# Optimization experiments

Hardware: AMD Instinct MI355X
Metric: run time of the kernel (lower is better)

## Reference

```python
import jax, jax.numpy as jnp
import numpy as np

B, S, D = 2, 2048, 2048
H, DH = 16, 128          # n_heads, head_dim
HFF = 8192               # hidden_dim (SwiGLU)
EPS = 1e-5               # layer_norm_eps passed to AdvancedRMSNorm


def setup_inputs() -> dict:
    key = jax.random.key(0)
    ks = jax.random.split(key, 16)
    sd = lambda fan_in: 1.0 / np.sqrt(fan_in)
    inp = {
        "x": jax.random.normal(ks[0], (B, S, D), jnp.float32),
        # attention (torch Linear weights: [out, in])
        "q_w": jax.random.normal(ks[1], (D, D), jnp.float32) * sd(D),
        "k_w": jax.random.normal(ks[2], (D, D), jnp.float32) * sd(D),
        "v_w": jax.random.normal(ks[3], (D, D), jnp.float32) * sd(D),
        "o_w": jax.random.normal(ks[4], (D, D), jnp.float32) * sd(D),
        "temp": jnp.ones((H, 1, 1), jnp.float32),  # learnable per-head temperature
        # RMSNorm scales
        "ln1_w": jnp.ones((D,), jnp.float32),
        "ln2_w": jnp.ones((D,), jnp.float32),
        # SwiGLU
        "gate_w": jax.random.normal(ks[5], (HFF, D), jnp.float32) * sd(D),
        "up_w": jax.random.normal(ks[6], (HFF, D), jnp.float32) * sd(D),
        "gate2_w": jax.random.normal(ks[7], (HFF, D), jnp.float32) * sd(D),
        "down_w": jax.random.normal(ks[8], (D, HFF), jnp.float32) * sd(HFF),
        # gated residual connections (Linear with bias)
        "ag_w": jax.random.normal(ks[9], (D, D), jnp.float32) * sd(D),
        "ag_b": jnp.zeros((D,), jnp.float32),
        "fg_w": jax.random.normal(ks[10], (D, D), jnp.float32) * sd(D),
        "fg_b": jnp.zeros((D,), jnp.float32),
    }
    return inp


def _rmsnorm(x, w):
    rms = jnp.sqrt(jnp.mean(x * x, axis=-1, keepdims=True) + EPS)
    return w * (x / rms)


def _l2norm(x):
    # F.normalize(dim=-1): x / max(||x||_2, 1e-12)
    n = jnp.sqrt(jnp.sum(x * x, axis=-1, keepdims=True))
    return x / jnp.maximum(n, 1e-12)


def _block(x, q_w, k_w, v_w, o_w, temp, ln1_w, ln2_w,
           gate_w, up_w, gate2_w, down_w, ag_w, ag_b, fg_w, fg_b):
    # --- cosine-sim attention sublayer ---
    residual = x
    h = _rmsnorm(x, ln1_w)
    q = (h @ q_w.T).reshape(B, S, H, DH).transpose(0, 2, 1, 3)  # [B,H,S,DH]
    k = (h @ k_w.T).reshape(B, S, H, DH).transpose(0, 2, 1, 3)
    v = (h @ v_w.T).reshape(B, S, H, DH).transpose(0, 2, 1, 3)
    q = _l2norm(q)
    k = _l2norm(k)
    scores = jnp.einsum("bhqd,bhkd->bhqk", q, k) * temp  # temp [H,1,1] broadcasts
    causal = jnp.triu(jnp.ones((S, S), bool), k=1)
    scores = jnp.where(causal, -jnp.inf, scores)
    attn = jax.nn.softmax(scores, axis=-1)
    out = jnp.einsum("bhqk,bhkd->bhqd", attn, v)
    out = out.transpose(0, 2, 1, 3).reshape(B, S, D)
    attn_out = out @ o_w.T
    # gated residual: sigmoid(W a + b)*a + (1-g)*residual
    g = jax.nn.sigmoid(attn_out @ ag_w.T + ag_b)
    x = g * attn_out + (1.0 - g) * residual
    # --- SwiGLU sublayer ---
    residual = x
    h = _rmsnorm(x, ln2_w)
    gate = jax.nn.silu(h @ gate_w.T)
    up = h @ up_w.T
    gate2 = jax.nn.sigmoid(h @ gate2_w.T)
    ffn_out = (gate * up * gate2) @ down_w.T
    g = jax.nn.sigmoid(ffn_out @ fg_w.T + fg_b)
    return g * ffn_out + (1.0 - g) * residual


def reference(x, q_w, k_w, v_w, o_w, temp, ln1_w, ln2_w,
              gate_w, up_w, gate2_w, down_w, ag_w, ag_b, fg_w, fg_b):
    return _block(x, q_w, k_w, v_w, o_w, temp, ln1_w, ln2_w,
                  gate_w, up_w, gate2_w, down_w, ag_w, ag_b, fg_w, fg_b)
```

## Files before the change

### kernel.cpp

```cpp
#include <hip/hip_runtime.h>

typedef unsigned short u16;
typedef unsigned int u32;
using bf16x8 = __attribute__((ext_vector_type(8))) short;
using f32x4  = __attribute__((ext_vector_type(4))) float;

#define EPS 1e-5f

__device__ __forceinline__ u16 f2bf(float f) {
    union { float f; u32 u; } v; v.f = f;
    u32 r = v.u + 0x7FFFu + ((v.u >> 16) & 1u);
    return (u16)(r >> 16);
}
__device__ __forceinline__ float bf2f(u16 u) {
    union { u32 u; float f; } v; v.u = ((u32)u) << 16;
    return v.f;
}
__device__ __forceinline__ void gl16(const void* g, void* s) {
    __builtin_amdgcn_global_load_lds(
        (const __attribute__((address_space(1))) u32*)g,
        (__attribute__((address_space(3))) u32*)s, 16, 0, 0);
}
__device__ __forceinline__ float sigm(float x) { return 1.f / (1.f + __expf(-x)); }

__global__ void conv_bf16(const float* __restrict__ src, u16* __restrict__ dst, int n4) {
    int i = blockIdx.x * 256 + threadIdx.x;
    if (i >= n4) return;
    float4 v = reinterpret_cast<const float4*>(src)[i];
    u32 lo = (u32)f2bf(v.x) | ((u32)f2bf(v.y) << 16);
    u32 hi = (u32)f2bf(v.z) | ((u32)f2bf(v.w) << 16);
    reinterpret_cast<uint2*>(dst)[i] = make_uint2(lo, hi);
}

__global__ void conv3_bf16(const float* __restrict__ s0, const float* __restrict__ s1,
                           const float* __restrict__ s2, u16* __restrict__ d0,
                           u16* __restrict__ d1, u16* __restrict__ d2, int n4) {
    int i = blockIdx.x * 256 + threadIdx.x;
    if (i >= n4) return;
    const float* src = (blockIdx.y == 0) ? s0 : (blockIdx.y == 1) ? s1 : s2;
    u16* dst = (blockIdx.y == 0) ? d0 : (blockIdx.y == 1) ? d1 : d2;
    float4 v = reinterpret_cast<const float4*>(src)[i];
    u32 lo = (u32)f2bf(v.x) | ((u32)f2bf(v.y) << 16);
    u32 hi = (u32)f2bf(v.z) | ((u32)f2bf(v.w) << 16);
    reinterpret_cast<uint2*>(dst)[i] = make_uint2(lo, hi);
}

__global__ void rmsnorm_k(const float* __restrict__ x, const float* __restrict__ wt,
                          u16* __restrict__ out) {
    __shared__ float red[4];
    const int row = blockIdx.x, t = threadIdx.x;
    const float* xr = x + (size_t)row * 2048;
    float4 v0 = *reinterpret_cast<const float4*>(&xr[t * 8]);
    float4 v1 = *reinterpret_cast<const float4*>(&xr[t * 8 + 4]);
    float ss = v0.x*v0.x + v0.y*v0.y + v0.z*v0.z + v0.w*v0.w
             + v1.x*v1.x + v1.y*v1.y + v1.z*v1.z + v1.w*v1.w;
#pragma unroll
    for (int d = 1; d < 64; d <<= 1) ss += __shfl_xor(ss, d);
    if ((t & 63) == 0) red[t >> 6] = ss;
    __syncthreads();
    const float tot = red[0] + red[1] + red[2] + red[3];
    const float s = 1.f / sqrtf(tot * (1.f / 2048.f) + EPS);
    float4 w0 = *reinterpret_cast<const float4*>(&wt[t * 8]);
    float4 w1 = *reinterpret_cast<const float4*>(&wt[t * 8 + 4]);
    u32 o[4];
    o[0] = (u32)f2bf(v0.x * s * w0.x) | ((u32)f2bf(v0.y * s * w0.y) << 16);
    o[1] = (u32)f2bf(v0.z * s * w0.z) | ((u32)f2bf(v0.w * s * w0.w) << 16);
    o[2] = (u32)f2bf(v1.x * s * w1.x) | ((u32)f2bf(v1.y * s * w1.y) << 16);
    o[3] = (u32)f2bf(v1.z * s * w1.z) | ((u32)f2bf(v1.w * s * w1.w) << 16);
    *reinterpret_cast<uint4*>(&out[(size_t)row * 2048 + t * 8]) =
        make_uint4(o[0], o[1], o[2], o[3]);
}

__global__ void qk_l2norm(u16* __restrict__ qkv, const float* __restrict__ temp) {
    const int wid = blockIdx.x * 4 + (threadIdx.x >> 6);
    const int l = threadIdx.x & 63;
    const int n = wid >> 5;
    const int rem = wid & 31;
    const int which = rem >> 4;
    const int h = rem & 15;
    u16* p = qkv + (size_t)n * 6144 + which * 2048 + h * 128 + l * 2;
    u32 v = *reinterpret_cast<const u32*>(p);
    float f0 = bf2f((u16)(v & 0xffff)), f1 = bf2f((u16)(v >> 16));
    float ss = f0 * f0 + f1 * f1;
#pragma unroll
    for (int d = 1; d < 64; d <<= 1) ss += __shfl_xor(ss, d);
    float sc = 1.f / fmaxf(sqrtf(ss), 1e-12f);
    if (which == 0) sc *= temp[h];
    *reinterpret_cast<u32*>(p) = (u32)f2bf(f0 * sc) | ((u32)f2bf(f1 * sc) << 16);
}

template <int EPI>
__global__ void gemm_bt(const u16* __restrict__ A, const u16* __restrict__ B,
                        float* __restrict__ outF, u16* __restrict__ outB,
                        const float* __restrict__ bias, const float* __restrict__ addend,
                        const float* __restrict__ resid, float* __restrict__ outG,
                        int M, int N, int K, int ldc) {
    __shared__ u16 as_[128 * 32];
    __shared__ u16 bs_[128 * 32];
    const int nbn = N >> 7;
    const int nwg = (M >> 7) * nbn;
    {
    }
    const int orig = blockIdx.x;
    const int q8 = nwg >> 3, r8 = nwg & 7;
    const int xcd = orig & 7, lin = orig >> 3;
    const int wgid = (xcd < r8 ? xcd * (q8 + 1) : r8 * (q8 + 1) + (xcd - r8) * q8) + lin;
    const int g = wgid / (nbn << 3);
    const int rem = wgid - g * (nbn << 3);
    const int bn = rem >> 3;
    const int bm = (g << 3) + (rem & 7);

    const int t = threadIdx.x;
    const int w = t >> 6, l = t & 63;
    const int wr = w >> 1, wc = w & 1;
    const int lr = l & 15, lg = l >> 4;
    f32x4 acc[4][4];
#pragma unroll
    for (int i = 0; i < 4; i++)
#pragma unroll
        for (int j = 0; j < 4; j++) acc[i][j] = (f32x4){0.f, 0.f, 0.f, 0.f};

    const int r0 = t >> 2;
    const int c0 = (t & 3) << 3;
    const u16* aG = A + (size_t)(bm * 128 + r0) * K + c0;
    const u16* bG = B + (size_t)(bn * 128 + r0) * K + c0;
    const size_t step64 = (size_t)64 * K;
    u16* as0 = &as_[t * 8]; u16* as1 = &as_[2048 + t * 8];
    u16* bs0 = &bs_[t * 8]; u16* bs1 = &bs_[2048 + t * 8];

    for (int kt = 0; kt < K; kt += 32) {
        __syncthreads();
        gl16(aG + kt, as0);
        gl16(aG + step64 + kt, as1);
        gl16(bG + kt, bs0);
        gl16(bG + step64 + kt, bs1);
        __syncthreads();
        bf16x8 af[4], bf[4];
#pragma unroll
        for (int i = 0; i < 4; i++)
            af[i] = *reinterpret_cast<const bf16x8*>(&as_[(wr * 64 + i * 16 + lr) * 32 + lg * 8]);
#pragma unroll
        for (int j = 0; j < 4; j++)
            bf[j] = *reinterpret_cast<const bf16x8*>(&bs_[(wc * 64 + j * 16 + lr) * 32 + lg * 8]);
#pragma unroll
        for (int i = 0; i < 4; i++)
#pragma unroll
            for (int j = 0; j < 4; j++)
                acc[i][j] = __builtin_amdgcn_mfma_f32_16x16x32_bf16(af[i], bf[j], acc[i][j], 0, 0, 0);
    }
#pragma unroll
    for (int i = 0; i < 4; i++) {
        const int row = bm * 128 + wr * 64 + i * 16 + lg * 4;
#pragma unroll
        for (int j = 0; j < 4; j++) {
            const int col = bn * 128 + wc * 64 + j * 16 + lr;
#pragma unroll
            for (int q = 0; q < 4; q++) {
                const size_t idx = (size_t)(row + q) * ldc + col;
                const float v = acc[i][j][q];
                if (EPI == 0) {
                    outB[idx] = f2bf(v);
                } else if (EPI == 1) {
                    outF[idx] = v;
                    outB[idx] = f2bf(v);
                } else {
                    const float g2 = sigm(v + bias[col]);
                    outG[idx] = g2 * addend[idx] + (1.f - g2) * resid[idx];
                }
            }
        }
    }
}

#define VSWZ(dh) (((((dh) >> 3) ^ (dh)) & 7) << 4)
__global__ __launch_bounds__(512) void flash_attn(const u16* __restrict__ qkv,
                                                  u16* __restrict__ out) {
    __shared__ u16 klds[2][64 * 128];
    __shared__ u16 vlds[2][128 * 64];
    __shared__ u16 plds[8][16 * 64];
    const int t = threadIdx.x, w = t >> 6, l = t & 63;
    const int lr = l & 15, lg = l >> 4;
    const int b0 = blockIdx.x;
    const int xcd = b0 & 7, i0 = b0 >> 3;
    const int bh = ((i0 & 3) << 3) | xcd;
    const int p = i0 >> 2;
    const int b = bh >> 4, h = bh & 15;
    const size_t base = (size_t)b * 2048;
    const int sr0 = t >> 4;
    const int sc0 = (t & 15) << 3;

    uint4 kreg0, kreg1, vreg0, vreg1;

#define STAGE_LOAD(KT) do {                                                          \
        const size_t gg = (base + (size_t)(KT) * 64 + sr0) * 6144 + h * 128 + sc0;   \
        kreg0 = *reinterpret_cast<const uint4*>(&qkv[gg + 2048]);                    \
        vreg0 = *reinterpret_cast<const uint4*>(&qkv[gg + 4096]);                    \
        kreg1 = *reinterpret_cast<const uint4*>(&qkv[gg + 32 * 6144 + 2048]);        \
        vreg1 = *reinterpret_cast<const uint4*>(&qkv[gg + 32 * 6144 + 4096]);        \
    } while (0)

#define STAGE_WRITE(BUF) do {                                                                     \
        char* kb = (char*)&klds[BUF][0];                                                          \
        char* vb = (char*)&vlds[BUF][0];                                                          \
        *reinterpret_cast<uint4*>(kb + ((sr0 * 256 + sc0 * 2) ^ ((sr0 & 7) << 4))) = kreg0;       \
        *reinterpret_cast<uint4*>(kb + (((sr0 + 32) * 256 + sc0 * 2) ^ ((sr0 & 7) << 4))) = kreg1;\
        union { uint4 u; u16 s[8]; } vv;                                                          \
        vv.u = vreg0;                                                                             \
        _Pragma("unroll")                                                                         \
        for (int jj = 0; jj < 8; jj++) {                                                          \
            const int dh = sc0 + jj;                                                              \
            *reinterpret_cast<u16*>(vb + ((dh * 128 + sr0 * 2) ^ VSWZ(dh))) = vv.s[jj];           \
        }                                                                                         \
        vv.u = vreg1;                                                                             \
        _Pragma("unroll")                                                                         \
        for (int jj = 0; jj < 8; jj++) {                                                          \
            const int dh = sc0 + jj;                                                              \
            *reinterpret_cast<u16*>(vb + ((dh * 128 + (sr0 + 32) * 2) ^ VSWZ(dh))) = vv.s[jj];    \
        }                                                                                         \
    } while (0)

    for (int phase = 0; phase < 2; ++phase) {
        const int qt = phase ? (15 - p) : p;
        const int last = 2 * qt + 1;
        const int qrow = qt * 128 + w * 16 + lr;
        const int qr0 = qt * 128 + w * 16 + lg * 4;
        bf16x8 qf[4];
#pragma unroll
        for (int kk = 0; kk < 4; kk++)
            qf[kk] = *reinterpret_cast<const bf16x8*>(
                &qkv[(base + qrow) * 6144 + h * 128 + kk * 32 + lg * 8]);
        f32x4 o[8];
#pragma unroll
        for (int i = 0; i < 8; i++) o[i] = (f32x4){0.f, 0.f, 0.f, 0.f};
        float m[4] = {-1e30f, -1e30f, -1e30f, -1e30f};
        float ls[4] = {0.f, 0.f, 0.f, 0.f};

        STAGE_LOAD(0);
        int cur = 0;
        STAGE_WRITE(0);
        __syncthreads();

        for (int kt = 0; kt <= last; ++kt) {
            if (kt < last) STAGE_LOAD(kt + 1);
            const char* kb = (const char*)&klds[cur][0];
            const char* vb = (const char*)&vlds[cur][0];
            f32x4 s[4];
#pragma unroll
            for (int nf = 0; nf < 4; nf++) {
                f32x4 a = (f32x4){0.f, 0.f, 0.f, 0.f};
                const int kv = nf * 16 + lr;
#pragma unroll
                for (int kk = 0; kk < 4; kk++) {
                    bf16x8 kf = *reinterpret_cast<const bf16x8*>(
                        kb + ((kv * 256 + kk * 64 + lg * 16) ^ ((kv & 7) << 4)));
                    a = __builtin_amdgcn_mfma_f32_16x16x32_bf16(qf[kk], kf, a, 0, 0, 0);
                }
                s[nf] = a;
            }
            if (kt >= 2 * qt) {
#pragma unroll
                for (int nf = 0; nf < 4; nf++) {
                    const int kvi = kt * 64 + nf * 16 + lr;
#pragma unroll
                    for (int q = 0; q < 4; q++)
                        if (kvi > qr0 + q) s[nf][q] = -1e30f;
                }
            }
            float mx[4] = {-1e30f, -1e30f, -1e30f, -1e30f};
#pragma unroll
            for (int nf = 0; nf < 4; nf++)
#pragma unroll
                for (int q = 0; q < 4; q++) mx[q] = fmaxf(mx[q], s[nf][q]);
#pragma unroll
            for (int q = 0; q < 4; q++) {
#pragma unroll
                for (int d = 1; d < 16; d <<= 1) mx[q] = fmaxf(mx[q], __shfl_xor(mx[q], d));
            }
            float fac[4], rs[4];
#pragma unroll
            for (int q = 0; q < 4; q++) {
                const float mn = fmaxf(m[q], mx[q]);
                fac[q] = __expf(m[q] - mn);
                m[q] = mn;
                rs[q] = 0.f;
            }
#pragma unroll
            for (int nf = 0; nf < 4; nf++) {
#pragma unroll
                for (int q = 0; q < 4; q++) {
                    const float pv = __expf(s[nf][q] - m[q]);
                    s[nf][q] = pv;
                    rs[q] += pv;
                }
            }
#pragma unroll
            for (int nf = 0; nf < 4; nf++) {
                const int col = nf * 16 + lr;
#pragma unroll
                for (int q = 0; q < 4; q++) {
                    const int row = lg * 4 + q;
                    *reinterpret_cast<u16*>((char*)&plds[w][0] +
                        ((row * 128 + col * 2) ^ ((row & 7) << 4))) = f2bf(s[nf][q]);
                }
            }
#pragma unroll
            for (int q = 0; q < 4; q++) {
#pragma unroll
                for (int d = 1; d < 16; d <<= 1) rs[q] += __shfl_xor(rs[q], d);
                ls[q] = ls[q] * fac[q] + rs[q];
            }
#pragma unroll
            for (int nf2 = 0; nf2 < 8; nf2++)
#pragma unroll
                for (int q = 0; q < 4; q++) o[nf2][q] *= fac[q];
#pragma unroll
            for (int ks = 0; ks < 2; ks++) {
                bf16x8 pf = *reinterpret_cast<const bf16x8*>((char*)&plds[w][0] +
                    ((lr * 128 + ks * 64 + lg * 16) ^ ((lr & 7) << 4)));
#pragma unroll
                for (int nf2 = 0; nf2 < 8; nf2++) {
                    const int dh = nf2 * 16 + lr;
                    bf16x8 vf = *reinterpret_cast<const bf16x8*>(
                        vb + ((dh * 128 + ks * 64 + lg * 16) ^ VSWZ(dh)));
                    o[nf2] = __builtin_amdgcn_mfma_f32_16x16x32_bf16(pf, vf, o[nf2], 0, 0, 0);
                }
            }
            if (kt < last) STAGE_WRITE(cur ^ 1);
            __syncthreads();
            cur ^= 1;
        }
#pragma unroll
        for (int nf2 = 0; nf2 < 8; nf2++) {
            const int col = h * 128 + nf2 * 16 + lr;
#pragma unroll
            for (int q = 0; q < 4; q++) {
                const float v = o[nf2][q] / ls[q];
                out[(base + qr0 + q) * 2048 + col] = f2bf(v);
            }
        }
        __syncthreads();
    }
#undef STAGE_LOAD
#undef STAGE_WRITE
}

__global__ void swiglu_comb(const u16* __restrict__ f3, u16* __restrict__ comb) {
    const size_t u = (size_t)blockIdx.x * 256 + threadIdx.x;
    const size_t n = u >> 8;
    const int f = (int)(u & 255) << 3;
    const u16* gp = f3 + n * 6144 + f;
    union { uint4 q; u16 s[8]; } g, up, g2;
    g.q  = *reinterpret_cast<const uint4*>(gp);
    up.q = *reinterpret_cast<const uint4*>(gp + 2048);
    g2.q = *reinterpret_cast<const uint4*>(gp + 4096);
    u32 r[4];
#pragma unroll
    for (int i = 0; i < 4; i++) {
        float a0 = bf2f(g.s[2 * i]),     a1 = bf2f(g.s[2 * i + 1]);
        float b0 = bf2f(up.s[2 * i]),    b1 = bf2f(up.s[2 * i + 1]);
        float c0 = bf2f(g2.s[2 * i]),    c1 = bf2f(g2.s[2 * i + 1]);
        float r0 = a0 * sigm(a0) * b0 * sigm(c0);
        float r1 = a1 * sigm(a1) * b1 * sigm(c1);
        r[i] = (u32)f2bf(r0) | ((u32)f2bf(r1) << 16);
    }
    *reinterpret_cast<uint4*>(comb + n * 8192 + f) = make_uint4(r[0], r[1], r[2], r[3]);
}

extern "C" void kernel_launch(void* const* d_in, const int* in_sizes, int n_in,
                              void* d_out, int out_size, void* d_ws, size_t ws_size,
                              hipStream_t stream) {
    const float* x      = (const float*)d_in[0];
    const float* q_w    = (const float*)d_in[1];
    const float* k_w    = (const float*)d_in[2];
    const float* v_w    = (const float*)d_in[3];
    const float* o_w    = (const float*)d_in[4];
    const float* temp   = (const float*)d_in[5];
    const float* ln1_w  = (const float*)d_in[6];
    const float* ln2_w  = (const float*)d_in[7];
    const float* gate_w = (const float*)d_in[8];
    const float* up_w   = (const float*)d_in[9];
    const float* gate2_w= (const float*)d_in[10];
    const float* down_w = (const float*)d_in[11];
    const float* ag_w   = (const float*)d_in[12];
    const float* ag_b   = (const float*)d_in[13];
    const float* fg_w   = (const float*)d_in[14];
    const float* fg_b   = (const float*)d_in[15];

    char* ws = (char*)d_ws;
    u16*  Wbuf = (u16*)(ws);
    u16*  hbuf = (u16*)(ws + 33554432);
    float* x1  = (float*)(ws + 50331648);
    u16*  combo= (u16*)(ws + 83886080);
    char* E    = ws + 150994944;
    char* F    = ws + 201326592;
    u16*  ffb  = (u16*)(ws + 234881024);

    u16*   qkvact = (u16*)E;
    float* aof    = (float*)E;
    u16*   aob    = (u16*)(E + 33554432);
    u16*   ffn3q  = (u16*)E;
    u16*   attnb  = (u16*)F;
    float* fff    = (float*)F;

    float* outp = (float*)d_out;
    const size_t DD = 2048ull * 2048ull;
    const int cg_d = (int)(DD / 4) / 256;

    hipLaunchKernelGGL(rmsnorm_k, dim3(4096), dim3(256), 0, stream, x, ln1_w, hbuf);

    hipLaunchKernelGGL(conv3_bf16, dim3(cg_d, 3), dim3(256), 0, stream,
                       q_w, k_w, v_w, Wbuf, Wbuf + DD, Wbuf + 2 * DD, (int)(DD / 4));
    hipLaunchKernelGGL((gemm_bt<0>), dim3(32 * 48), dim3(256), 0, stream,
                       hbuf, Wbuf, (float*)nullptr, qkvact,
                       (const float*)nullptr, (const float*)nullptr, (const float*)nullptr,
                       (float*)nullptr, 4096, 6144, 2048, 6144);

    hipLaunchKernelGGL(qk_l2norm, dim3(32768), dim3(256), 0, stream, qkvact, temp);

    hipLaunchKernelGGL(flash_attn, dim3(256), dim3(512), 0, stream, qkvact, attnb);

    hipLaunchKernelGGL(conv_bf16, dim3(cg_d), dim3(256), 0, stream, o_w, Wbuf, (int)(DD / 4));
    hipLaunchKernelGGL((gemm_bt<1>), dim3(32 * 16), dim3(256), 0, stream,
                       attnb, Wbuf, aof, aob,
                       (const float*)nullptr, (const float*)nullptr, (const float*)nullptr,
                       (float*)nullptr, 4096, 2048, 2048, 2048);

    hipLaunchKernelGGL(conv_bf16, dim3(cg_d), dim3(256), 0, stream, ag_w, Wbuf, (int)(DD / 4));
    hipLaunchKernelGGL((gemm_bt<2>), dim3(32 * 16), dim3(256), 0, stream,
                       aob, Wbuf, (float*)nullptr, (u16*)nullptr,
                       ag_b, aof, x, x1, 4096, 2048, 2048, 2048);

    hipLaunchKernelGGL(rmsnorm_k, dim3(4096), dim3(256), 0, stream, x1, ln2_w, hbuf);

    for (int qd = 0; qd < 4; qd++) {
        const size_t wofs = (size_t)qd * 2048 * 2048;
        hipLaunchKernelGGL(conv3_bf16, dim3(cg_d, 3), dim3(256), 0, stream,
                           gate_w + wofs, up_w + wofs, gate2_w + wofs,
                           Wbuf, Wbuf + 2048 * 2048, Wbuf + 2ull * 2048 * 2048, (int)(DD / 4));
        hipLaunchKernelGGL((gemm_bt<0>), dim3(32 * 48), dim3(256), 0, stream,
                           hbuf, Wbuf, (float*)nullptr, ffn3q,
                           (const float*)nullptr, (const float*)nullptr, (const float*)nullptr,
                           (float*)nullptr, 4096, 6144, 2048, 6144);
        hipLaunchKernelGGL(swiglu_comb, dim3(4096), dim3(256), 0, stream, ffn3q, combo + qd * 2048);
    }

    hipLaunchKernelGGL(conv_bf16, dim3(16384), dim3(256), 0, stream, down_w, Wbuf, (int)(2048ull * 8192 / 4));
    hipLaunchKernelGGL((gemm_bt<1>), dim3(32 * 16), dim3(256), 0, stream,
                       combo, Wbuf, fff, ffb,
                       (const float*)nullptr, (const float*)nullptr, (const float*)nullptr,
                       (float*)nullptr, 4096, 2048, 8192, 2048);

    hipLaunchKernelGGL(conv_bf16, dim3(cg_d), dim3(256), 0, stream, fg_w, Wbuf, (int)(DD / 4));
    hipLaunchKernelGGL((gemm_bt<2>), dim3(32 * 16), dim3(256), 0, stream,
                       ffb, Wbuf, (float*)nullptr, (u16*)nullptr,
                       fg_b, fff, x1, outp, 4096, 2048, 2048, 2048);
}
```

Baseline: 1.248 ms.

## Rewrite GEMM with 128x256 tiles, triple-buffered LDS pipeline and swizzled K=64 stages

Rewrites the bf16 GEMM to use 512-thread workgroups on 128x256 output tiles with K=64 stages. Direct-to-LDS loads go into a triple-buffered ring, and the next-next tile's loads are split into two phases interleaved with the MFMA halves. An XOR swizzle on the LDS layout avoids bank conflicts, and s_setprio raises wave priority around the MFMA bursts. The goal is to hide global-load latency behind compute and raise data reuse per tile, which the previous single-buffered loop with two syncthreads per 32-wide K step could not do. The cost is a large dynamic LDS footprint (144KB), one workgroup per CU, and fewer workgroups for the smaller GEMMs.

```diff
diff --git a/kernel.cpp b/kernel.cpp
--- a/kernel.cpp
+++ b/kernel.cpp
@@ -90,17 +90,15 @@
 }
 
 template <int EPI>
-__global__ void gemm_bt(const u16* __restrict__ A, const u16* __restrict__ B,
-                        float* __restrict__ outF, u16* __restrict__ outB,
-                        const float* __restrict__ bias, const float* __restrict__ addend,
-                        const float* __restrict__ resid, float* __restrict__ outG,
-                        int M, int N, int K, int ldc) {
-    __shared__ u16 as_[128 * 32];
-    __shared__ u16 bs_[128 * 32];
-    const int nbn = N >> 7;
+__global__ __launch_bounds__(512, 1)
+void gemm_bt(const u16* __restrict__ A, const u16* __restrict__ B,
+             float* __restrict__ outF, u16* __restrict__ outB,
+             const float* __restrict__ bias, const float* __restrict__ addend,
+             const float* __restrict__ resid, float* __restrict__ outG,
+             int M, int N, int K, int ldc) {
+    extern __shared__ u16 lds[];
+    const int nbn = N >> 8;
     const int nwg = (M >> 7) * nbn;
-    {
-    }
     const int orig = blockIdx.x;
     const int q8 = nwg >> 3, r8 = nwg & 7;
     const int xcd = orig & 7, lin = orig >> 3;
@@ -112,52 +110,117 @@
 
     const int t = threadIdx.x;
     const int w = t >> 6, l = t & 63;
-    const int wr = w >> 1, wc = w & 1;
+    const int wr = w >> 2, wc = w & 3;
     const int lr = l & 15, lg = l >> 4;
+    const int NT = K >> 6;
+
+    const int pr = t >> 3, ps = t & 7;
+    const int sg = ps ^ (pr & 7);
+    const u16* aSrc = A + (size_t)(bm * 128 + pr) * K + sg * 8;
+    const u16* bSrc = B + (size_t)(bn * 256 + pr) * K + sg * 8;
+    const size_t rowStep = (size_t)64 * K;
+
+#define STAGE_P0(TT, bi) do {                                                   \
+        u16* da = lds + (bi) * 24576 + t * 8;                                   \
+        gl16(aSrc + (size_t)(TT) * 64, da);                                     \
+        gl16(aSrc + rowStep + (size_t)(TT) * 64, da + 4096);                    \
+        gl16(bSrc + (size_t)(TT) * 64, lds + (bi) * 24576 + 8192 + t * 8);      \
+    } while (0)
+#define STAGE_P1(TT, bi) do {                                                   \
+        u16* db = lds + (bi) * 24576 + 8192 + t * 8;                            \
+        gl16(bSrc + rowStep + (size_t)(TT) * 64, db + 4096);                    \
+        gl16(bSrc + 2 * rowStep + (size_t)(TT) * 64, db + 8192);                \
+        gl16(bSrc + 3 * rowStep + (size_t)(TT) * 64, db + 12288);               \
+    } while (0)
+
     f32x4 acc[4][4];
 #pragma unroll
     for (int i = 0; i < 4; i++)
 #pragma unroll
         for (int j = 0; j < 4; j++) acc[i][j] = (f32x4){0.f, 0.f, 0.f, 0.f};
 
-    const int r0 = t >> 2;
-    const int c0 = (t & 3) << 3;
-    const u16* aG = A + (size_t)(bm * 128 + r0) * K + c0;
-    const u16* bG = B + (size_t)(bn * 128 + r0) * K + c0;
-    const size_t step64 = (size_t)64 * K;
-    u16* as0 = &as_[t * 8]; u16* as1 = &as_[2048 + t * 8];
-    u16* bs0 = &bs_[t * 8]; u16* bs1 = &bs_[2048 + t * 8];
-
-    for (int kt = 0; kt < K; kt += 32) {
-        __syncthreads();
-        gl16(aG + kt, as0);
-        gl16(aG + step64 + kt, as1);
-        gl16(bG + kt, bs0);
-        gl16(bG + step64 + kt, bs1);
-        __syncthreads();
-        bf16x8 af[4], bf[4];
-#pragma unroll
-        for (int i = 0; i < 4; i++)
-            af[i] = *reinterpret_cast<const bf16x8*>(&as_[(wr * 64 + i * 16 + lr) * 32 + lg * 8]);
-#pragma unroll
-        for (int j = 0; j < 4; j++)
-            bf[j] = *reinterpret_cast<const bf16x8*>(&bs_[(wc * 64 + j * 16 + lr) * 32 + lg * 8]);
-#pragma unroll
-        for (int i = 0; i < 4; i++)
-#pragma unroll
-            for (int j = 0; j < 4; j++)
-                acc[i][j] = __builtin_amdgcn_mfma_f32_16x16x32_bf16(af[i], bf[j], acc[i][j], 0, 0, 0);
+    const int xr = (lr & 7) << 4;
+    const int kof0 = ((lg) << 4) ^ xr;
+    const int kof1 = ((4 + lg) << 4) ^ xr;
+
+    STAGE_P0(0, 0); STAGE_P1(0, 0);
+    if (NT > 1) {
+        STAGE_P0(1, 1); STAGE_P1(1, 1);
+        asm volatile("s_waitcnt vmcnt(6)" ::: "memory");
+    } else {
+        asm volatile("s_waitcnt vmcnt(0)" ::: "memory");
     }
-#pragma unroll
-    for (int i = 0; i < 4; i++) {
-        const int row = bm * 128 + wr * 64 + i * 16 + lg * 4;
-#pragma unroll
-        for (int j = 0; j < 4; j++) {
-            const int col = bn * 128 + wc * 64 + j * 16 + lr;
+    __builtin_amdgcn_s_barrier();
+
+    for (int T = 0; T < NT; ++T) {
+        const int bi = T % 3;
+        const int sbi = (T + 2) % 3;
+        const bool st = (T + 2) < NT;
+        const char* bufA = (const char*)(lds + bi * 24576);
+        const char* bufB = bufA + 16384;
+        bf16x8 bf[4][2], af[2][2];
+#pragma unroll
+        for (int n = 0; n < 4; n++) {
+            const int rb = wc * 64 + n * 16 + lr;
+            bf[n][0] = *reinterpret_cast<const bf16x8*>(bufB + rb * 128 + kof0);
+            bf[n][1] = *reinterpret_cast<const bf16x8*>(bufB + rb * 128 + kof1);
+        }
+#pragma unroll
+        for (int m = 0; m < 2; m++) {
+            const int ra = wr * 64 + m * 16 + lr;
+            af[m][0] = *reinterpret_cast<const bf16x8*>(bufA + ra * 128 + kof0);
+            af[m][1] = *reinterpret_cast<const bf16x8*>(bufA + ra * 128 + kof1);
+        }
+        if (st) STAGE_P0(T + 2, sbi);
+        __builtin_amdgcn_s_barrier();
+        __builtin_amdgcn_s_setprio(1);
+#pragma unroll
+        for (int m = 0; m < 2; m++)
+#pragma unroll
+            for (int n = 0; n < 4; n++) {
+                acc[m][n] = __builtin_amdgcn_mfma_f32_16x16x32_bf16(af[m][0], bf[n][0], acc[m][n], 0, 0, 0);
+                acc[m][n] = __builtin_amdgcn_mfma_f32_16x16x32_bf16(af[m][1], bf[n][1], acc[m][n], 0, 0, 0);
+            }
+        __builtin_amdgcn_s_setprio(0);
+        __builtin_amdgcn_s_barrier();
+        bf16x8 ag[2][2];
+#pragma unroll
+        for (int m = 0; m < 2; m++) {
+            const int ra = wr * 64 + (m + 2) * 16 + lr;
+            ag[m][0] = *reinterpret_cast<const bf16x8*>(bufA + ra * 128 + kof0);
+            ag[m][1] = *reinterpret_cast<const bf16x8*>(bufA + ra * 128 + kof1);
+        }
+        if (st) STAGE_P1(T + 2, sbi);
+        __builtin_amdgcn_s_barrier();
+        __builtin_amdgcn_s_setprio(1);
+#pragma unroll
+        for (int m = 0; m < 2; m++)
+#pragma unroll
+            for (int n = 0; n < 4; n++) {
+                acc[m + 2][n] = __builtin_amdgcn_mfma_f32_16x16x32_bf16(ag[m][0], bf[n][0], acc[m + 2][n], 0, 0, 0);
+                acc[m + 2][n] = __builtin_amdgcn_mfma_f32_16x16x32_bf16(ag[m][1], bf[n][1], acc[m + 2][n], 0, 0, 0);
+            }
+        __builtin_amdgcn_s_setprio(0);
+        if (st) {
+            asm volatile("s_waitcnt vmcnt(6)" ::: "memory");
+        } else if (T + 1 < NT) {
+            asm volatile("s_waitcnt vmcnt(0)" ::: "memory");
+        }
+        __builtin_amdgcn_s_barrier();
+    }
+#undef STAGE_P0
+#undef STAGE_P1
+
+#pragma unroll
+    for (int m = 0; m < 4; m++) {
+        const int row = bm * 128 + wr * 64 + m * 16 + lg * 4;
+#pragma unroll
+        for (int n = 0; n < 4; n++) {
+            const int col = bn * 256 + wc * 64 + n * 16 + lr;
 #pragma unroll
             for (int q = 0; q < 4; q++) {
                 const size_t idx = (size_t)(row + q) * ldc + col;
-                const float v = acc[i][j][q];
+                const float v = acc[m][n][q];
                 if (EPI == 0) {
                     outB[idx] = f2bf(v);
                 } else if (EPI == 1) {
@@ -386,6 +449,14 @@
     const float* fg_w   = (const float*)d_in[14];
     const float* fg_b   = (const float*)d_in[15];
 
+    const int GEMM_LDS = 147456;
+    (void)hipFuncSetAttribute(reinterpret_cast<const void*>(&gemm_bt<0>),
+                              hipFuncAttributeMaxDynamicSharedMemorySize, GEMM_LDS);
+    (void)hipFuncSetAttribute(reinterpret_cast<const void*>(&gemm_bt<1>),
+                              hipFuncAttributeMaxDynamicSharedMemorySize, GEMM_LDS);
+    (void)hipFuncSetAttribute(reinterpret_cast<const void*>(&gemm_bt<2>),
+                              hipFuncAttributeMaxDynamicSharedMemorySize, GEMM_LDS);
+
     char* ws = (char*)d_ws;
     u16*  Wbuf = (u16*)(ws);
     u16*  hbuf = (u16*)(ws + 33554432);
@@ -405,12 +476,14 @@
     float* outp = (float*)d_out;
     const size_t DD = 2048ull * 2048ull;
     const int cg_d = (int)(DD / 4) / 256;
+    const int GRID_BIG = 32 * 24;
+    const int GRID_SM  = 32 * 8;
 
     hipLaunchKernelGGL(rmsnorm_k, dim3(4096), dim3(256), 0, stream, x, ln1_w, hbuf);
 
     hipLaunchKernelGGL(conv3_bf16, dim3(cg_d, 3), dim3(256), 0, stream,
                        q_w, k_w, v_w, Wbuf, Wbuf + DD, Wbuf + 2 * DD, (int)(DD / 4));
-    hipLaunchKernelGGL((gemm_bt<0>), dim3(32 * 48), dim3(256), 0, stream,
+    hipLaunchKernelGGL((gemm_bt<0>), dim3(GRID_BIG), dim3(512), GEMM_LDS, stream,
                        hbuf, Wbuf, (float*)nullptr, qkvact,
                        (const float*)nullptr, (const float*)nullptr, (const float*)nullptr,
                        (float*)nullptr, 4096, 6144, 2048, 6144);
@@ -420,13 +493,13 @@
     hipLaunchKernelGGL(flash_attn, dim3(256), dim3(512), 0, stream, qkvact, attnb);
 
     hipLaunchKernelGGL(conv_bf16, dim3(cg_d), dim3(256), 0, stream, o_w, Wbuf, (int)(DD / 4));
-    hipLaunchKernelGGL((gemm_bt<1>), dim3(32 * 16), dim3(256), 0, stream,
+    hipLaunchKernelGGL((gemm_bt<1>), dim3(GRID_SM), dim3(512), GEMM_LDS, stream,
                        attnb, Wbuf, aof, aob,
                        (const float*)nullptr, (const float*)nullptr, (const float*)nullptr,
                        (float*)nullptr, 4096, 2048, 2048, 2048);
 
     hipLaunchKernelGGL(conv_bf16, dim3(cg_d), dim3(256), 0, stream, ag_w, Wbuf, (int)(DD / 4));
-    hipLaunchKernelGGL((gemm_bt<2>), dim3(32 * 16), dim3(256), 0, stream,
+    hipLaunchKernelGGL((gemm_bt<2>), dim3(GRID_SM), dim3(512), GEMM_LDS, stream,
                        aob, Wbuf, (float*)nullptr, (u16*)nullptr,
                        ag_b, aof, x, x1, 4096, 2048, 2048, 2048);
 
@@ -437,7 +510,7 @@
         hipLaunchKernelGGL(conv3_bf16, dim3(cg_d, 3), dim3(256), 0, stream,
                            gate_w + wofs, up_w + wofs, gate2_w + wofs,
                            Wbuf, Wbuf + 2048 * 2048, Wbuf + 2ull * 2048 * 2048, (int)(DD / 4));
-        hipLaunchKernelGGL((gemm_bt<0>), dim3(32 * 48), dim3(256), 0, stream,
+        hipLaunchKernelGGL((gemm_bt<0>), dim3(GRID_BIG), dim3(512), GEMM_LDS, stream,
                            hbuf, Wbuf, (float*)nullptr, ffn3q,
                            (const float*)nullptr, (const float*)nullptr, (const float*)nullptr,
                            (float*)nullptr, 4096, 6144, 2048, 6144);
@@ -445,13 +518,13 @@
     }
 
     hipLaunchKernelGGL(conv_bf16, dim3(16384), dim3(256), 0, stream, down_w, Wbuf, (int)(2048ull * 8192 / 4));
-    hipLaunchKernelGGL((gemm_bt<1>), dim3(32 * 16), dim3(256), 0, stream,
+    hipLaunchKernelGGL((gemm_bt<1>), dim3(GRID_SM), dim3(512), GEMM_LDS, stream,
                        combo, Wbuf, fff, ffb,
                        (const float*)nullptr, (const float*)nullptr, (const float*)nullptr,
                        (float*)nullptr, 4096, 2048, 8192, 2048);
 
     hipLaunchKernelGGL(conv_bf16, dim3(cg_d), dim3(256), 0, stream, fg_w, Wbuf, (int)(DD / 4));
-    hipLaunchKernelGGL((gemm_bt<2>), dim3(32 * 16), dim3(256), 0, stream,
+    hipLaunchKernelGGL((gemm_bt<2>), dim3(GRID_SM), dim3(512), GEMM_LDS, stream,
                        ffb, Wbuf, (float*)nullptr, (u16*)nullptr,
                        fg_b, fff, x1, outp, 4096, 2048, 2048, 2048);
 }
```

Result: faster. 1.134 ms (-9.1%).
